# Optimization experiments

Hardware: AMD Instinct MI355X
Metric: run time of the kernel (lower is better)

## Reference

```python
import jax, jax.numpy as jnp
import numpy as np

D_MODEL, D_STATE, D_INNER, DT_RANK, K = 64, 16, 128, 4, 4
EPS = 1e-6  # RMSNorm eps


def setup_inputs() -> dict:
    key = jax.random.key(0)
    ks = jax.random.split(key, 12)
    B, L = 8, 4096
    s = 0.02
    x = jax.random.normal(ks[0], (B, L, D_MODEL), dtype=jnp.float32)
    w_norm = jnp.ones((D_MODEL,), jnp.float32)
    W_in = jax.random.normal(ks[1], (2 * D_INNER, D_MODEL), jnp.float32) * s
    b_in = jnp.zeros((2 * D_INNER,), jnp.float32)
    W_conv = jax.random.normal(ks[2], (D_INNER, D_INNER, K), jnp.float32) * s
    b_conv = jnp.zeros((D_INNER,), jnp.float32)
    W_xp = jax.random.normal(ks[3], (DT_RANK + 2 * D_STATE, D_INNER), jnp.float32) * s
    b_xp = jnp.zeros((DT_RANK + 2 * D_STATE,), jnp.float32)
    W_dt = jax.random.normal(ks[4], (D_INNER, DT_RANK), jnp.float32) * s
    b_dt = jnp.zeros((D_INNER,), jnp.float32)
    W_out = jax.random.normal(ks[5], (D_MODEL, D_INNER), jnp.float32) * s
    b_out = jnp.zeros((D_MODEL,), jnp.float32)
    A_log = jnp.log(jnp.tile(jnp.arange(1, D_STATE + 1, dtype=jnp.float32), (D_INNER, 1)))
    D_param = jnp.ones((D_INNER,), jnp.float32)
    return dict(x=x, w_norm=w_norm, W_in=W_in, b_in=b_in, W_conv=W_conv, b_conv=b_conv,
                W_xp=W_xp, b_xp=b_xp, W_dt=W_dt, b_dt=b_dt, W_out=W_out, b_out=b_out,
                A_log=A_log, D_param=D_param)


def _mamba_block(xn, W_in, b_in, W_conv, b_conv, W_xp, b_xp, W_dt, b_dt, W_out, b_out, A_log, D_param):
    B, L, _ = xn.shape
    xz = xn @ W_in.T + b_in                      # (B,L,2*d_inner)
    u, z = jnp.split(xz, 2, axis=-1)
    z = jax.nn.silu(z)
    # conv1d: NCH, causal-style pad (K-1) both sides then truncate to L
    uc = jax.lax.conv_general_dilated(
        u.transpose(0, 2, 1), W_conv, window_strides=(1,), padding=[(K - 1, K - 1)],
        dimension_numbers=("NCH", "OIH", "NCH"))[:, :, :L] + b_conv[None, :, None]
    u = jax.nn.silu(uc.transpose(0, 2, 1))       # (B,L,d_inner)
    xp = u @ W_xp.T + b_xp
    dt, Bm, Cm = jnp.split(xp, [DT_RANK, DT_RANK + D_STATE], axis=-1)
    delta = jax.nn.softplus(dt @ W_dt.T + b_dt)  # (B,L,d_inner)
    A = -jnp.exp(A_log)                          # (d_inner, n)
    A_bar = jnp.exp(jnp.einsum('bld,dn->bldn', delta, A))
    B_bar_x = jnp.einsum('bld,bln,bld->bldn', delta, Bm, u)

    def step(h, inp):
        a, bx, c = inp                           # (B,d,n),(B,d,n),(B,n)
        h = a * h + bx
        y = jnp.einsum('bdn,bn->bd', h, c)
        return h, y

    h0 = jnp.zeros((B, D_INNER, D_STATE), xn.dtype)
    xs = (A_bar.transpose(1, 0, 2, 3), B_bar_x.transpose(1, 0, 2, 3), Cm.transpose(1, 0, 2))
    _, ys = jax.lax.scan(step, h0, xs)           # (L,B,d_inner)
    y = ys.transpose(1, 0, 2) + D_param * u
    y = y * z
    return y @ W_out.T + b_out


def reference(x, w_norm, W_in, b_in, W_conv, b_conv, W_xp, b_xp, W_dt, b_dt, W_out, b_out, A_log, D_param):
    xn = x * jax.lax.rsqrt(jnp.mean(x * x, axis=-1, keepdims=True) + EPS) * w_norm
    return x + _mamba_block(xn, W_in, b_in, W_conv, b_conv, W_xp, b_xp, W_dt, b_dt, W_out, b_out, A_log, D_param)
```

## Files before the change

kernel.cpp:

```cpp
#include <hip/hip_runtime.h>
#include <math.h>

#define D_MODEL 64
#define D_STATE 16
#define D_INNER 128
#define DT_RANK 4
#define BB 8
#define LL 4096
#define NTOK (BB*LL)
#define EPSV 1e-6f
#define NCHUNK 64
#define LC (LL/NCHUNK)
#define PAD 136

typedef __attribute__((ext_vector_type(8))) short bf16x8;
typedef __attribute__((ext_vector_type(4))) float f32x4;

__device__ __forceinline__ float sig_(float v) { return 1.f / (1.f + __expf(-v)); }
__device__ __forceinline__ float softplus_(float v) {
    return (v > 20.f) ? v : __logf(1.f + __expf(v));
}
__device__ __forceinline__ unsigned short f2bf(float x) {
    unsigned int u = __float_as_uint(x);
    u += 0x7fff + ((u >> 16) & 1);
    return (unsigned short)(u >> 16);
}
__device__ __forceinline__ float bf2f(unsigned short u) {
    return __uint_as_float(((unsigned int)u) << 16);
}

__global__ __launch_bounds__(256) void pack_all(
    const float* __restrict__ W_in, const float* __restrict__ w_norm,
    const float* __restrict__ W_conv, const float* __restrict__ W_xp,
    const float* __restrict__ W_out,
    unsigned short* __restrict__ Win_bf, unsigned short* __restrict__ Bp,
    unsigned short* __restrict__ Wxp_bf, unsigned short* __restrict__ Wout_bf)
{
    int i = blockIdx.x * 256 + threadIdx.x;
    if (i < 16384) {
        Win_bf[i] = f2bf(W_in[i] * w_norm[i & 63]);
    } else if (i < 81920) {
        int j = i - 16384;
        int kk = j >> 14, o = (j >> 7) & 127, c = j & 127;
        Bp[j] = f2bf(W_conv[o * 512 + c * 4 + kk]);
    } else if (i < 88064) {
        int j = i - 81920;
        Wxp_bf[j] = ((j >> 7) < 36) ? f2bf(W_xp[j]) : (unsigned short)0;
    } else if (i < 96256) {
        int j = i - 88064;
        Wout_bf[j] = f2bf(W_out[j]);
    }
}

__global__ __launch_bounds__(256) void k1_fused(
    const float* __restrict__ x, const unsigned short* __restrict__ Win_bf,
    const float* __restrict__ b_in,
    unsigned short* __restrict__ u_bf, unsigned short* __restrict__ z_bf)
{
    __shared__ unsigned short axs[64 * 72];
    int tid = threadIdx.x;
    int tb = blockIdx.x * 64;
    {
        int t = tid >> 2, qt = tid & 3;
        float4 v[4];
        float ss = 0.f;
        #pragma unroll
        for (int j = 0; j < 4; ++j) {
            v[j] = *(const float4*)&x[(tb + t) * 64 + qt * 16 + j * 4];
            ss += v[j].x*v[j].x + v[j].y*v[j].y + v[j].z*v[j].z + v[j].w*v[j].w;
        }
        ss += __shfl_xor(ss, 1, 64);
        ss += __shfl_xor(ss, 2, 64);
        float r = rsqrtf(ss * (1.f / 64.f) + EPSV);
        unsigned short tmp[16];
        #pragma unroll
        for (int j = 0; j < 4; ++j) {
            tmp[4*j+0] = f2bf(v[j].x * r); tmp[4*j+1] = f2bf(v[j].y * r);
            tmp[4*j+2] = f2bf(v[j].z * r); tmp[4*j+3] = f2bf(v[j].w * r);
        }
        *(bf16x8*)&axs[t * 72 + qt * 16]     = *(bf16x8*)&tmp[0];
        *(bf16x8*)&axs[t * 72 + qt * 16 + 8] = *(bf16x8*)&tmp[8];
    }
    __syncthreads();
    int wave = tid >> 6, lane = tid & 63;
    int quad = lane >> 4, l16 = lane & 15;
    f32x4 acc[16];
    #pragma unroll
    for (int nt = 0; nt < 16; ++nt) acc[nt] = (f32x4){0.f, 0.f, 0.f, 0.f};
    bf16x8 a0 = *(const bf16x8*)&axs[(wave * 16 + l16) * 72 + quad * 8];
    bf16x8 a1 = *(const bf16x8*)&axs[(wave * 16 + l16) * 72 + 32 + quad * 8];
    #pragma unroll
    for (int nt = 0; nt < 16; ++nt) {
        bf16x8 b0 = *(const bf16x8*)&Win_bf[(nt * 16 + l16) * 64 + quad * 8];
        bf16x8 b1 = *(const bf16x8*)&Win_bf[(nt * 16 + l16) * 64 + 32 + quad * 8];
        acc[nt] = __builtin_amdgcn_mfma_f32_16x16x32_bf16(a0, b0, acc[nt], 0, 0, 0);
        acc[nt] = __builtin_amdgcn_mfma_f32_16x16x32_bf16(a1, b1, acc[nt], 0, 0, 0);
    }
    #pragma unroll
    for (int nt = 0; nt < 16; ++nt) {
        int o = nt * 16 + l16;
        float bo = b_in[o];
        #pragma unroll
        for (int r = 0; r < 4; ++r) {
            int t = tb + wave * 16 + quad * 4 + r;
            float v = acc[nt][r] + bo;
            if (o < 128) u_bf[t * 128 + o] = f2bf(v);
            else         z_bf[t * 128 + (o - 128)] = f2bf(v * sig_(v));
        }
    }
}

__global__ __launch_bounds__(256) void k2k3_fused(
    const unsigned short* __restrict__ u_bf, const unsigned short* __restrict__ Bp,
    const float* __restrict__ b_conv,
    const unsigned short* __restrict__ Wxp_bf, const float* __restrict__ b_xp,
    const float* __restrict__ W_dt, const float* __restrict__ b_dt,
    unsigned short* __restrict__ u_cbf, float* __restrict__ delta,
    float* __restrict__ Bm, float* __restrict__ Cm)
{
    __shared__ unsigned short uls[64 * PAD];
    __shared__ float dts[64][4];
    __shared__ float Wd[512];
    __shared__ float bds[128];
    int tid = threadIdx.x;
    if (tid < 128) *(float4*)&Wd[tid * 4] = *(const float4*)&W_dt[tid * 4];
    else if (tid < 160) *(float4*)&bds[(tid - 128) * 4] = *(const float4*)&b_dt[(tid - 128) * 4];
    int wave = tid >> 6, lane = tid & 63;
    int quad = lane >> 4, l16 = lane & 15;
    int tb = blockIdx.x * 64;
    int bbase = tb & ~4095;
    int t0 = tb + wave * 16;
    f32x4 acc[8];
    #pragma unroll
    for (int og = 0; og < 8; ++og) acc[og] = (f32x4){0.f, 0.f, 0.f, 0.f};
    int row_base = t0 + l16 - 3;
    #pragma unroll
    for (int kk = 0; kk < 4; ++kk) {
        int row = row_base + kk;
        #pragma unroll
        for (int cs = 0; cs < 4; ++cs) {
            int kbase = cs * 32 + quad * 8;
            bf16x8 a = {0,0,0,0,0,0,0,0};
            if (row >= bbase)
                a = *(const bf16x8*)&u_bf[row * 128 + kbase];
            #pragma unroll
            for (int og = 0; og < 8; ++og) {
                bf16x8 b = *(const bf16x8*)&Bp[kk * 16384 + (og * 16 + l16) * 128 + kbase];
                acc[og] = __builtin_amdgcn_mfma_f32_16x16x32_bf16(a, b, acc[og], 0, 0, 0);
            }
        }
    }
    #pragma unroll
    for (int og = 0; og < 8; ++og) {
        int o = og * 16 + l16;
        float bc = b_conv[o];
        #pragma unroll
        for (int r = 0; r < 4; ++r) {
            int tloc = wave * 16 + quad * 4 + r;
            float v = acc[og][r] + bc;
            unsigned short ub = f2bf(v * sig_(v));
            u_cbf[(tb + tloc) * 128 + o] = ub;
            uls[tloc * PAD + o] = ub;
        }
    }
    __syncthreads();
    f32x4 xacc[3];
    #pragma unroll
    for (int nt = 0; nt < 3; ++nt) xacc[nt] = (f32x4){0.f, 0.f, 0.f, 0.f};
    #pragma unroll
    for (int cs = 0; cs < 4; ++cs) {
        int kbase = cs * 32 + quad * 8;
        bf16x8 a = *(const bf16x8*)&uls[(wave * 16 + l16) * PAD + kbase];
        #pragma unroll
        for (int nt = 0; nt < 3; ++nt) {
            bf16x8 b = *(const bf16x8*)&Wxp_bf[(nt * 16 + l16) * 128 + kbase];
            xacc[nt] = __builtin_amdgcn_mfma_f32_16x16x32_bf16(a, b, xacc[nt], 0, 0, 0);
        }
    }
    #pragma unroll
    for (int nt = 0; nt < 3; ++nt) {
        int j = nt * 16 + l16;
        float bx = (j < 36) ? b_xp[j] : 0.f;
        #pragma unroll
        for (int r = 0; r < 4; ++r) {
            int tloc = wave * 16 + quad * 4 + r;
            int t = tb + tloc;
            float val = xacc[nt][r] + bx;
            if (j < 4)       dts[tloc][j] = val;
            else if (j < 20) Bm[t * 16 + (j - 4)]  = val;
            else if (j < 36) Cm[t * 16 + (j - 20)] = val;
        }
    }
    __syncthreads();
    int tokloc = tid >> 2, dgrp = tid & 3;
    float dt0 = dts[tokloc][0], dt1 = dts[tokloc][1],
          dt2 = dts[tokloc][2], dt3 = dts[tokloc][3];
    int g = tb + tokloc;
    #pragma unroll
    for (int d4 = 0; d4 < 8; ++d4) {
        int d = dgrp * 32 + d4 * 4;
        float4 w0 = *(const float4*)&Wd[(d + 0) * 4];
        float4 w1 = *(const float4*)&Wd[(d + 1) * 4];
        float4 w2 = *(const float4*)&Wd[(d + 2) * 4];
        float4 w3 = *(const float4*)&Wd[(d + 3) * 4];
        float4 bdv = *(const float4*)&bds[d];
        float4 r;
        r.x = softplus_(bdv.x + dt0*w0.x + dt1*w0.y + dt2*w0.z + dt3*w0.w);
        r.y = softplus_(bdv.y + dt0*w1.x + dt1*w1.y + dt2*w1.z + dt3*w1.w);
        r.z = softplus_(bdv.z + dt0*w2.x + dt1*w2.y + dt2*w2.z + dt3*w2.w);
        r.w = softplus_(bdv.w + dt0*w3.x + dt1*w3.y + dt2*w3.z + dt3*w3.w);
        *(float4*)&delta[g * 128 + d] = r;
    }
}

__global__ __launch_bounds__(256) void k4a_chunk(
    const float* __restrict__ delta, const unsigned short* __restrict__ u_cbf,
    const float* __restrict__ Bm, const float* __restrict__ A_log,
    float* __restrict__ P, float* __restrict__ Q)
{
    __shared__ float dls[LC * 64];
    __shared__ unsigned short uls[LC * 64];
    __shared__ float bls[LC * 16];
    int bid = blockIdx.x;
    int b = bid >> 7, c = (bid >> 1) & 63, half = bid & 1;
    int tid = threadIdx.x, lane = tid & 63;
    int g0 = b * LL + c * LC;
    int d0 = half * 64;
    for (int i = tid; i < LC * 16; i += 256) {
        int row = i >> 4, q = i & 15;
        *(float4*)&dls[row * 64 + q * 4] =
            *(const float4*)&delta[(g0 + row) * 128 + d0 + q * 4];
    }
    for (int i = tid; i < LC * 8; i += 256) {
        int row = i >> 3, q = i & 7;
        *(float4*)&uls[row * 64 + q * 8] =
            *(const float4*)&u_cbf[(g0 + row) * 128 + d0 + q * 8];
    }
    for (int i = tid; i < LC * 4; i += 256) {
        int row = i >> 2, q = i & 3;
        *(float4*)&bls[row * 16 + q * 4] =
            *(const float4*)&Bm[(g0 + row) * 16 + q * 4];
    }
    int dloc = (tid >> 6) * 16 + (lane >> 2);
    int d = d0 + dloc;
    int ng = lane & 3;
    float4 Av = *(const float4*)&A_log[d * 16 + ng * 4];
    float A0 = -__expf(Av.x), A1 = -__expf(Av.y), A2 = -__expf(Av.z), A3 = -__expf(Av.w);
    float P0=1.f,P1=1.f,P2=1.f,P3=1.f, Q0=0.f,Q1=0.f,Q2=0.f,Q3=0.f;
    __syncthreads();
    for (int t = 0; t < LC; ++t) {
        float dl = dls[t * 64 + dloc];
        float uu = bf2f(uls[t * 64 + dloc]);
        float4 bm = *(const float4*)&bls[t * 16 + ng * 4];
        float du = dl * uu;
        float a0 = __expf(dl * A0), a1 = __expf(dl * A1),
              a2 = __expf(dl * A2), a3 = __expf(dl * A3);
        P0 *= a0; P1 *= a1; P2 *= a2; P3 *= a3;
        Q0 = a0 * Q0 + du * bm.x; Q1 = a1 * Q1 + du * bm.y;
        Q2 = a2 * Q2 + du * bm.z; Q3 = a3 * Q3 + du * bm.w;
    }
    int idx = (b * NCHUNK + c) * 2048 + d * 16 + ng * 4;
    *(float4*)&P[idx] = (float4){P0, P1, P2, P3};
    *(float4*)&Q[idx] = (float4){Q0, Q1, Q2, Q3};
}

__global__ __launch_bounds__(256) void k4b_carry(
    const float* __restrict__ P, const float* __restrict__ Q, float* __restrict__ Hinit)
{
    int tid = blockIdx.x * 256 + threadIdx.x;
    int b = tid >> 11, dn = tid & 2047;
    float carry = 0.f;
    for (int c = 0; c < NCHUNK; ++c) {
        int idx = (b * NCHUNK + c) * 2048 + dn;
        Hinit[idx] = carry;
        carry = P[idx] * carry + Q[idx];
    }
}

__global__ __launch_bounds__(256) void k4c_scan(
    const float* __restrict__ delta, const unsigned short* __restrict__ u_cbf,
    const float* __restrict__ Bm, const float* __restrict__ Cm,
    const unsigned short* __restrict__ z_bf, const float* __restrict__ A_log,
    const float* __restrict__ D_param, const float* __restrict__ Hinit,
    unsigned short* __restrict__ y_bf)
{
    __shared__ float dls[LC * 64];
    __shared__ unsigned short uls[LC * 64];
    __shared__ float bls[LC * 16];
    __shared__ float cls[LC * 16];
    __shared__ unsigned short zls[LC * 64];
    int bid = blockIdx.x;
    int b = bid >> 7, c = (bid >> 1) & 63, half = bid & 1;
    int tid = threadIdx.x, lane = tid & 63;
    int g0 = b * LL + c * LC;
    int d0 = half * 64;
    for (int i = tid; i < LC * 16; i += 256) {
        int row = i >> 4, q = i & 15;
        *(float4*)&dls[row * 64 + q * 4] =
            *(const float4*)&delta[(g0 + row) * 128 + d0 + q * 4];
    }
    for (int i = tid; i < LC * 8; i += 256) {
        int row = i >> 3, q = i & 7;
        *(float4*)&uls[row * 64 + q * 8] =
            *(const float4*)&u_cbf[(g0 + row) * 128 + d0 + q * 8];
        *(float4*)&zls[row * 64 + q * 8] =
            *(const float4*)&z_bf[(g0 + row) * 128 + d0 + q * 8];
    }
    for (int i = tid; i < LC * 4; i += 256) {
        int row = i >> 2, q = i & 3;
        *(float4*)&bls[row * 16 + q * 4] =
            *(const float4*)&Bm[(g0 + row) * 16 + q * 4];
        *(float4*)&cls[row * 16 + q * 4] =
            *(const float4*)&Cm[(g0 + row) * 16 + q * 4];
    }
    int dloc = (tid >> 6) * 16 + (lane >> 2);
    int d = d0 + dloc;
    int ng = lane & 3;
    float4 Av = *(const float4*)&A_log[d * 16 + ng * 4];
    float A0 = -__expf(Av.x), A1 = -__expf(Av.y), A2 = -__expf(Av.z), A3 = -__expf(Av.w);
    float4 h = *(const float4*)&Hinit[(b * NCHUNK + c) * 2048 + d * 16 + ng * 4];
    float Dp = D_param[d];
    __syncthreads();
    for (int t = 0; t < LC; ++t) {
        float dl = dls[t * 64 + dloc];
        float uu = bf2f(uls[t * 64 + dloc]);
        float4 bm = *(const float4*)&bls[t * 16 + ng * 4];
        float4 cm = *(const float4*)&cls[t * 16 + ng * 4];
        float du = dl * uu;
        float a0 = __expf(dl * A0), a1 = __expf(dl * A1),
              a2 = __expf(dl * A2), a3 = __expf(dl * A3);
        h.x = a0 * h.x + du * bm.x; h.y = a1 * h.y + du * bm.y;
        h.z = a2 * h.z + du * bm.z; h.w = a3 * h.w + du * bm.w;
        float yv = h.x * cm.x + h.y * cm.y + h.z * cm.z + h.w * cm.w;
        yv += __shfl_xor(yv, 1, 64);
        yv += __shfl_xor(yv, 2, 64);
        if (ng == 0) {
            float y = yv + Dp * uu;
            y *= bf2f(zls[t * 64 + dloc]);
            y_bf[(g0 + t) * 128 + d] = f2bf(y);
        }
    }
}

__global__ __launch_bounds__(256) void k5_outproj_mfma(
    const unsigned short* __restrict__ y_bf, const unsigned short* __restrict__ Wout_bf,
    const float* __restrict__ b_out, const float* __restrict__ x,
    float* __restrict__ out)
{
    int tid = threadIdx.x;
    int wave = tid >> 6, lane = tid & 63;
    int quad = lane >> 4, l16 = lane & 15;
    int t0 = blockIdx.x * 64 + wave * 16;
    f32x4 acc[4];
    #pragma unroll
    for (int nt = 0; nt < 4; ++nt) acc[nt] = (f32x4){0.f, 0.f, 0.f, 0.f};
    #pragma unroll
    for (int cs = 0; cs < 4; ++cs) {
        int kbase = cs * 32 + quad * 8;
        bf16x8 a = *(const bf16x8*)&y_bf[(t0 + l16) * 128 + kbase];
        #pragma unroll
        for (int nt = 0; nt < 4; ++nt) {
            bf16x8 b = *(const bf16x8*)&Wout_bf[(nt * 16 + l16) * 128 + kbase];
            acc[nt] = __builtin_amdgcn_mfma_f32_16x16x32_bf16(a, b, acc[nt], 0, 0, 0);
        }
    }
    #pragma unroll
    for (int nt = 0; nt < 4; ++nt) {
        int m = nt * 16 + l16;
        float bo = b_out[m];
        #pragma unroll
        for (int r = 0; r < 4; ++r) {
            int t = t0 + quad * 4 + r;
            out[t * 64 + m] = acc[nt][r] + bo + x[t * 64 + m];
        }
    }
}

extern "C" void kernel_launch(void* const* d_in, const int* in_sizes, int n_in,
                              void* d_out, int out_size, void* d_ws, size_t ws_size,
                              hipStream_t stream)
{
    const float* x       = (const float*)d_in[0];
    const float* w_norm  = (const float*)d_in[1];
    const float* W_in    = (const float*)d_in[2];
    const float* b_in    = (const float*)d_in[3];
    const float* W_conv  = (const float*)d_in[4];
    const float* b_conv  = (const float*)d_in[5];
    const float* W_xp    = (const float*)d_in[6];
    const float* b_xp    = (const float*)d_in[7];
    const float* W_dt    = (const float*)d_in[8];
    const float* b_dt    = (const float*)d_in[9];
    const float* W_out   = (const float*)d_in[10];
    const float* b_out   = (const float*)d_in[11];
    const float* A_log   = (const float*)d_in[12];
    const float* D_param = (const float*)d_in[13];
    float* ws = (float*)d_ws;

    unsigned short* u_bf = (unsigned short*)ws;
    unsigned short* y_bf = (unsigned short*)ws;
    unsigned short* z_bf = (unsigned short*)(ws + 2097152);
    unsigned short* u_cbf= (unsigned short*)(ws + 4194304);
    float* delta  = ws + 6291456;
    float* Bm     = ws + 10485760;
    float* Cm     = ws + 11010048;
    float* P      = ws + 11534336;
    float* Q      = ws + 12582912;
    float* Hinit  = ws + 13631488;
    unsigned short* Bp      = (unsigned short*)(ws + 14680064);
    unsigned short* Wxp_bf  = (unsigned short*)(ws + 14712832);
    unsigned short* Wout_bf = (unsigned short*)(ws + 14715904);
    unsigned short* Win_bf  = (unsigned short*)(ws + 14720000);
    float* out    = (float*)d_out;

    pack_all<<<376, 256, 0, stream>>>(W_in, w_norm, W_conv, W_xp, W_out,
                                      Win_bf, Bp, Wxp_bf, Wout_bf);
    k1_fused<<<512, 256, 0, stream>>>(x, Win_bf, b_in, u_bf, z_bf);
    k2k3_fused<<<512, 256, 0, stream>>>(u_bf, Bp, b_conv, Wxp_bf, b_xp,
                                        W_dt, b_dt, u_cbf, delta, Bm, Cm);
    k4a_chunk<<<1024, 256, 0, stream>>>(delta, u_cbf, Bm, A_log, P, Q);
    k4b_carry<<<64, 256, 0, stream>>>(P, Q, Hinit);
    k4c_scan<<<1024, 256, 0, stream>>>(delta, u_cbf, Bm, Cm, z_bf, A_log,
                                       D_param, Hinit, y_bf);
    k5_outproj_mfma<<<512, 256, 0, stream>>>(y_bf, Wout_bf, b_out, x, out);
}
```

Before: 199.9 us.

## Fuse chunk-local scan summary into conv/xproj kernel via shared memory

The separate k4a_chunk kernel is folded into the conv+x_proj kernel. Delta, B and the conv output already sit in LDS, so the per-chunk P/Q products are computed there without re-reading delta, u_cbf and Bm from global memory, and one launch is removed. Each thread now handles 8 states instead of 4, and 512 blocks do the work 1024 blocks did before. This raises LDS use and register pressure and serializes the scan after the projection inside one block.

```diff
diff --git a/kernel.cpp b/kernel.cpp
--- a/kernel.cpp
+++ b/kernel.cpp
@@ -12,6 +12,7 @@
 #define NCHUNK 64
 #define LC (LL/NCHUNK)
 #define PAD 136
+#define PADF 132
 
 typedef __attribute__((ext_vector_type(8))) short bf16x8;
 typedef __attribute__((ext_vector_type(4))) float f32x4;
@@ -110,15 +111,19 @@
     }
 }
 
-__global__ __launch_bounds__(256) void k2k3_fused(
+__global__ __launch_bounds__(256) void k2k3a_fused(
     const unsigned short* __restrict__ u_bf, const unsigned short* __restrict__ Bp,
     const float* __restrict__ b_conv,
     const unsigned short* __restrict__ Wxp_bf, const float* __restrict__ b_xp,
     const float* __restrict__ W_dt, const float* __restrict__ b_dt,
+    const float* __restrict__ A_log,
     unsigned short* __restrict__ u_cbf, float* __restrict__ delta,
-    float* __restrict__ Bm, float* __restrict__ Cm)
+    float* __restrict__ Bm, float* __restrict__ Cm,
+    float* __restrict__ P, float* __restrict__ Q)
 {
     __shared__ unsigned short uls[64 * PAD];
+    __shared__ float dls[64 * PADF];
+    __shared__ float bls[64 * 16];
     __shared__ float dts[64][4];
     __shared__ float Wd[512];
     __shared__ float bds[128];
@@ -186,82 +191,74 @@
             int tloc = wave * 16 + quad * 4 + r;
             int t = tb + tloc;
             float val = xacc[nt][r] + bx;
-            if (j < 4)       dts[tloc][j] = val;
-            else if (j < 20) Bm[t * 16 + (j - 4)]  = val;
-            else if (j < 36) Cm[t * 16 + (j - 20)] = val;
+            if (j < 4) {
+                dts[tloc][j] = val;
+            } else if (j < 20) {
+                Bm[t * 16 + (j - 4)] = val;
+                bls[tloc * 16 + (j - 4)] = val;
+            } else if (j < 36) {
+                Cm[t * 16 + (j - 20)] = val;
+            }
         }
     }
     __syncthreads();
-    int tokloc = tid >> 2, dgrp = tid & 3;
-    float dt0 = dts[tokloc][0], dt1 = dts[tokloc][1],
-          dt2 = dts[tokloc][2], dt3 = dts[tokloc][3];
-    int g = tb + tokloc;
-    #pragma unroll
-    for (int d4 = 0; d4 < 8; ++d4) {
-        int d = dgrp * 32 + d4 * 4;
-        float4 w0 = *(const float4*)&Wd[(d + 0) * 4];
-        float4 w1 = *(const float4*)&Wd[(d + 1) * 4];
-        float4 w2 = *(const float4*)&Wd[(d + 2) * 4];
-        float4 w3 = *(const float4*)&Wd[(d + 3) * 4];
-        float4 bdv = *(const float4*)&bds[d];
-        float4 r;
-        r.x = softplus_(bdv.x + dt0*w0.x + dt1*w0.y + dt2*w0.z + dt3*w0.w);
-        r.y = softplus_(bdv.y + dt0*w1.x + dt1*w1.y + dt2*w1.z + dt3*w1.w);
-        r.z = softplus_(bdv.z + dt0*w2.x + dt1*w2.y + dt2*w2.z + dt3*w2.w);
-        r.w = softplus_(bdv.w + dt0*w3.x + dt1*w3.y + dt2*w3.z + dt3*w3.w);
-        *(float4*)&delta[g * 128 + d] = r;
-    }
-}
-
-__global__ __launch_bounds__(256) void k4a_chunk(
-    const float* __restrict__ delta, const unsigned short* __restrict__ u_cbf,
-    const float* __restrict__ Bm, const float* __restrict__ A_log,
-    float* __restrict__ P, float* __restrict__ Q)
-{
-    __shared__ float dls[LC * 64];
-    __shared__ unsigned short uls[LC * 64];
-    __shared__ float bls[LC * 16];
-    int bid = blockIdx.x;
-    int b = bid >> 7, c = (bid >> 1) & 63, half = bid & 1;
-    int tid = threadIdx.x, lane = tid & 63;
-    int g0 = b * LL + c * LC;
-    int d0 = half * 64;
-    for (int i = tid; i < LC * 16; i += 256) {
-        int row = i >> 4, q = i & 15;
-        *(float4*)&dls[row * 64 + q * 4] =
-            *(const float4*)&delta[(g0 + row) * 128 + d0 + q * 4];
-    }
-    for (int i = tid; i < LC * 8; i += 256) {
-        int row = i >> 3, q = i & 7;
-        *(float4*)&uls[row * 64 + q * 8] =
-            *(const float4*)&u_cbf[(g0 + row) * 128 + d0 + q * 8];
-    }
-    for (int i = tid; i < LC * 4; i += 256) {
-        int row = i >> 2, q = i & 3;
-        *(float4*)&bls[row * 16 + q * 4] =
-            *(const float4*)&Bm[(g0 + row) * 16 + q * 4];
-    }
-    int dloc = (tid >> 6) * 16 + (lane >> 2);
-    int d = d0 + dloc;
-    int ng = lane & 3;
-    float4 Av = *(const float4*)&A_log[d * 16 + ng * 4];
-    float A0 = -__expf(Av.x), A1 = -__expf(Av.y), A2 = -__expf(Av.z), A3 = -__expf(Av.w);
-    float P0=1.f,P1=1.f,P2=1.f,P3=1.f, Q0=0.f,Q1=0.f,Q2=0.f,Q3=0.f;
+    {
+        int tokloc = tid >> 2, dgrp = tid & 3;
+        float dt0 = dts[tokloc][0], dt1 = dts[tokloc][1],
+              dt2 = dts[tokloc][2], dt3 = dts[tokloc][3];
+        int g = tb + tokloc;
+        #pragma unroll
+        for (int d4 = 0; d4 < 8; ++d4) {
+            int d = dgrp * 32 + d4 * 4;
+            float4 w0 = *(const float4*)&Wd[(d + 0) * 4];
+            float4 w1 = *(const float4*)&Wd[(d + 1) * 4];
+            float4 w2 = *(const float4*)&Wd[(d + 2) * 4];
+            float4 w3 = *(const float4*)&Wd[(d + 3) * 4];
+            float4 bdv = *(const float4*)&bds[d];
+            float4 r;
+            r.x = softplus_(bdv.x + dt0*w0.x + dt1*w0.y + dt2*w0.z + dt3*w0.w);
+            r.y = softplus_(bdv.y + dt0*w1.x + dt1*w1.y + dt2*w1.z + dt3*w1.w);
+            r.z = softplus_(bdv.z + dt0*w2.x + dt1*w2.y + dt2*w2.z + dt3*w2.w);
+            r.w = softplus_(bdv.w + dt0*w3.x + dt1*w3.y + dt2*w3.z + dt3*w3.w);
+            *(float4*)&delta[g * 128 + d] = r;
+            *(float4*)&dls[tokloc * PADF + d] = r;
+        }
+    }
     __syncthreads();
-    for (int t = 0; t < LC; ++t) {
-        float dl = dls[t * 64 + dloc];
-        float uu = bf2f(uls[t * 64 + dloc]);
-        float4 bm = *(const float4*)&bls[t * 16 + ng * 4];
-        float du = dl * uu;
-        float a0 = __expf(dl * A0), a1 = __expf(dl * A1),
-              a2 = __expf(dl * A2), a3 = __expf(dl * A3);
-        P0 *= a0; P1 *= a1; P2 *= a2; P3 *= a3;
-        Q0 = a0 * Q0 + du * bm.x; Q1 = a1 * Q1 + du * bm.y;
-        Q2 = a2 * Q2 + du * bm.z; Q3 = a3 * Q3 + du * bm.w;
-    }
-    int idx = (b * NCHUNK + c) * 2048 + d * 16 + ng * 4;
-    *(float4*)&P[idx] = (float4){P0, P1, P2, P3};
-    *(float4*)&Q[idx] = (float4){Q0, Q1, Q2, Q3};
+    {
+        int d = tid >> 1;
+        int nb = (tid & 1) * 8;
+        float4 Av0 = *(const float4*)&A_log[d * 16 + nb];
+        float4 Av1 = *(const float4*)&A_log[d * 16 + nb + 4];
+        float A0 = -__expf(Av0.x), A1 = -__expf(Av0.y),
+              A2 = -__expf(Av0.z), A3 = -__expf(Av0.w);
+        float A4 = -__expf(Av1.x), A5 = -__expf(Av1.y),
+              A6 = -__expf(Av1.z), A7 = -__expf(Av1.w);
+        float P0=1.f,P1=1.f,P2=1.f,P3=1.f,P4=1.f,P5=1.f,P6=1.f,P7=1.f;
+        float Q0=0.f,Q1=0.f,Q2=0.f,Q3=0.f,Q4=0.f,Q5=0.f,Q6=0.f,Q7=0.f;
+        for (int t = 0; t < LC; ++t) {
+            float dl = dls[t * PADF + d];
+            float uu = bf2f(uls[t * PAD + d]);
+            float4 bm0 = *(const float4*)&bls[t * 16 + nb];
+            float4 bm1 = *(const float4*)&bls[t * 16 + nb + 4];
+            float du = dl * uu;
+            float a0 = __expf(dl * A0), a1 = __expf(dl * A1),
+                  a2 = __expf(dl * A2), a3 = __expf(dl * A3);
+            float a4 = __expf(dl * A4), a5 = __expf(dl * A5),
+                  a6 = __expf(dl * A6), a7 = __expf(dl * A7);
+            P0 *= a0; P1 *= a1; P2 *= a2; P3 *= a3;
+            P4 *= a4; P5 *= a5; P6 *= a6; P7 *= a7;
+            Q0 = a0 * Q0 + du * bm0.x; Q1 = a1 * Q1 + du * bm0.y;
+            Q2 = a2 * Q2 + du * bm0.z; Q3 = a3 * Q3 + du * bm0.w;
+            Q4 = a4 * Q4 + du * bm1.x; Q5 = a5 * Q5 + du * bm1.y;
+            Q6 = a6 * Q6 + du * bm1.z; Q7 = a7 * Q7 + du * bm1.w;
+        }
+        int idx = blockIdx.x * 2048 + d * 16 + nb;
+        *(float4*)&P[idx]     = (float4){P0, P1, P2, P3};
+        *(float4*)&P[idx + 4] = (float4){P4, P5, P6, P7};
+        *(float4*)&Q[idx]     = (float4){Q0, Q1, Q2, Q3};
+        *(float4*)&Q[idx + 4] = (float4){Q4, Q5, Q6, Q7};
+    }
 }
 
 __global__ __launch_bounds__(256) void k4b_carry(
@@ -415,9 +412,9 @@
     pack_all<<<376, 256, 0, stream>>>(W_in, w_norm, W_conv, W_xp, W_out,
                                       Win_bf, Bp, Wxp_bf, Wout_bf);
     k1_fused<<<512, 256, 0, stream>>>(x, Win_bf, b_in, u_bf, z_bf);
-    k2k3_fused<<<512, 256, 0, stream>>>(u_bf, Bp, b_conv, Wxp_bf, b_xp,
-                                        W_dt, b_dt, u_cbf, delta, Bm, Cm);
-    k4a_chunk<<<1024, 256, 0, stream>>>(delta, u_cbf, Bm, A_log, P, Q);
+    k2k3a_fused<<<512, 256, 0, stream>>>(u_bf, Bp, b_conv, Wxp_bf, b_xp,
+                                         W_dt, b_dt, A_log,
+                                         u_cbf, delta, Bm, Cm, P, Q);
     k4b_carry<<<64, 256, 0, stream>>>(P, Q, Hinit);
     k4c_scan<<<1024, 256, 0, stream>>>(delta, u_cbf, Bm, Cm, z_bf, A_log,
                                        D_param, Hinit, y_bf);
```

Result: no change. 196.9 us (-1.5%).
